# Kernel optimization log

Hardware: AMD Instinct MI355X
Metric: run time of the kernel (lower is better)

Reference implementation:

```python
import jax, jax.numpy as jnp
import numpy as np

NEG_INF = -9e15  # matches torch's -9000000000000000.0 fill


def setup_inputs() -> dict:
    key = jax.random.key(0)
    k1, k2, k3 = jax.random.split(key, 3)
    N, F = 8192, 256
    x = jax.random.normal(k1, (N, F), dtype=jnp.float32)
    adj = jax.random.randint(k2, (N, N), 0, 2, dtype=jnp.int32)
    # weight init mimics uniform(-stdv, stdv), stdv = 1/sqrt(F)
    stdv = 1.0 / np.sqrt(F)
    weight = jax.random.uniform(k3, (F, F), dtype=jnp.float32, minval=-stdv, maxval=stdv)
    return {"x": x, "adj": adj, "weight": weight}


def reference(x, adj, weight):
    # h: [N, F]
    h = x @ weight
    # e: [N, N] pairwise scores
    e = jnp.einsum("nf,mf->nm", h, h)
    masked = jnp.where(adj > 0, e, jnp.float32(NEG_INF))
    return jax.nn.softmax(masked, axis=1)
```

## Files before the change

kernel.cpp:

```cpp
#include <hip/hip_runtime.h>

typedef _Float16 f16;
typedef _Float16 f16x8 __attribute__((ext_vector_type(8)));
typedef float f32x4 __attribute__((ext_vector_type(4)));
typedef unsigned int u32;

#define NN 8192
#define FF 256
#define MASK_NEG -1.0e30f

__device__ __forceinline__ void gload_lds16(const void* gsrc, void* ldst) {
    __builtin_amdgcn_global_load_lds(
        (const __attribute__((address_space(1))) u32*)gsrc,
        (__attribute__((address_space(3))) u32*)ldst, 16, 0, 0);
}

__global__ void k0_wt(const float* __restrict__ w, f16* __restrict__ wt) {
    int n = blockIdx.x;
    int k = threadIdx.x;
    wt[n * FF + k] = (f16)w[k * FF + n];
}

__global__ __launch_bounds__(256) void k1_h(const float* __restrict__ x,
                                            const f16* __restrict__ wt,
                                            f16* __restrict__ h) {
    int tid = threadIdx.x;
    int wave = tid >> 6, lane = tid & 63, l15 = lane & 15, lg = lane >> 4;
    int rowBase = blockIdx.x * 32 + (wave & 1) * 16;
    int colBase = (wave >> 1) * 128;

    f16x8 afr[8];
    const float* xr = x + (size_t)(rowBase + l15) * FF + lg * 8;
#pragma unroll
    for (int kk = 0; kk < 8; ++kk) {
        float4 a0 = *(const float4*)(xr + kk * 32);
        float4 a1 = *(const float4*)(xr + kk * 32 + 4);
        f16x8 a;
        a[0] = (f16)a0.x; a[1] = (f16)a0.y; a[2] = (f16)a0.z; a[3] = (f16)a0.w;
        a[4] = (f16)a1.x; a[5] = (f16)a1.y; a[6] = (f16)a1.z; a[7] = (f16)a1.w;
        afr[kk] = a;
    }
#pragma unroll
    for (int cs = 0; cs < 8; ++cs) {
        int col = colBase + cs * 16 + l15;
        f32x4 acc = {0.f, 0.f, 0.f, 0.f};
        const f16* wr = wt + (size_t)col * FF + lg * 8;
#pragma unroll
        for (int kk = 0; kk < 8; ++kk) {
            f16x8 b = *(const f16x8*)(wr + kk * 32);
            acc = __builtin_amdgcn_mfma_f32_16x16x32_f16(afr[kk], b, acc, 0, 0, 0);
        }
#pragma unroll
        for (int r = 0; r < 4; ++r)
            h[(size_t)(rowBase + 4 * lg + r) * FF + col] = (f16)acc[r];
    }
}

__global__ __launch_bounds__(256) void k2a(const f16* __restrict__ h,
                                           const int* __restrict__ adj,
                                           u32* __restrict__ maskbits,
                                           float* __restrict__ pm,
                                           float* __restrict__ ps) {
    __shared__ __align__(16) f16 tile[128 * 256];
    int bid = blockIdx.x;
    int rb = bid >> 2, split = bid & 3;
    int tid = threadIdx.x;
    int wave = tid >> 6, lane = tid & 63, l15 = lane & 15, lg = lane >> 4;
    int rowBase = rb * 64 + wave * 16;

    f16x8 afr[8];
    {
        const f16* ar = h + (size_t)(rowBase + l15) * FF + lg * 8;
#pragma unroll
        for (int kk = 0; kk < 8; ++kk) afr[kk] = *(const f16x8*)(ar + kk * 32);
    }
    float m[4], s[4];
#pragma unroll
    for (int r = 0; r < 4; ++r) { m[r] = MASK_NEG; s[r] = 0.f; }

    int colStart = split * 2048;
    int prow = rowBase + (lane >> 2);
    int pwc = lane & 3;
    const int* adjRow = adj + (size_t)prow * NN;

    int4 aj[8];
    {
        const int4* ap = (const int4*)(adjRow + colStart + pwc * 32);
#pragma unroll
        for (int k = 0; k < 8; ++k) aj[k] = ap[k];
    }

    for (int it = 0; it < 16; ++it) {
        int c0 = colStart + it * 128;
        __syncthreads();
#pragma unroll
        for (int i = 0; i < 16; ++i) {
            int cbase = i * 256 + wave * 64;
            int c = cbase + lane;
            int row = c >> 5;
            int kb = (c & 31) * 16;
            const char* src = (const char*)h + (size_t)(c0 + row) * 512
                              + (kb ^ ((row & 7) << 4));
            gload_lds16(src, (char*)tile + (size_t)cbase * 16);
        }
        __syncthreads();

        u32 word = 0;
#pragma unroll
        for (int k = 0; k < 8; ++k) {
            word |= (aj[k].x > 0 ? 1u : 0u) << (k * 4);
            word |= (aj[k].y > 0 ? 1u : 0u) << (k * 4 + 1);
            word |= (aj[k].z > 0 ? 1u : 0u) << (k * 4 + 2);
            word |= (aj[k].w > 0 ? 1u : 0u) << (k * 4 + 3);
        }
        maskbits[(size_t)prow * 256 + (c0 >> 5) + pwc] = word;

        if (it + 1 < 16) {
            const int4* ap = (const int4*)(adjRow + c0 + 128 + pwc * 32);
#pragma unroll
            for (int k = 0; k < 8; ++k) aj[k] = ap[k];
        }

        f32x4 acc[8];
#pragma unroll
        for (int cs = 0; cs < 8; ++cs) {
            int trow = cs * 16 + l15;
            const char* tbase = (const char*)tile + trow * 512;
            int sw = (trow & 7) << 4;
            f32x4 a = {0.f, 0.f, 0.f, 0.f};
#pragma unroll
            for (int kk = 0; kk < 8; ++kk) {
                f16x8 b = *(const f16x8*)(tbase + ((kk * 64 + lg * 16) ^ sw));
                a = __builtin_amdgcn_mfma_f32_16x16x32_f16(afr[kk], b, a, 0, 0, 0);
            }
            acc[cs] = a;
        }

#pragma unroll
        for (int r = 0; r < 4; ++r) {
            int srcBase = 16 * lg + 4 * r;
            float vv[8];
            float tm = MASK_NEG;
#pragma unroll
            for (int wc = 0; wc < 4; ++wc) {
                u32 w = (u32)__shfl((int)word, srcBase + wc, 64);
                float v0 = ((w >> l15) & 1u) ? acc[wc * 2][r] : MASK_NEG;
                float v1 = ((w >> (16 + l15)) & 1u) ? acc[wc * 2 + 1][r] : MASK_NEG;
                vv[wc * 2] = v0;
                vv[wc * 2 + 1] = v1;
                tm = fmaxf(tm, fmaxf(v0, v1));
            }
            float mn = fmaxf(m[r], tm);
            float add = 0.f;
#pragma unroll
            for (int cs = 0; cs < 8; ++cs) add += __expf(vv[cs] - mn);
            s[r] = s[r] * __expf(m[r] - mn) + add;
            m[r] = mn;
        }
    }

#pragma unroll
    for (int off = 1; off < 16; off <<= 1) {
#pragma unroll
        for (int r = 0; r < 4; ++r) {
            float om = __shfl_xor(m[r], off);
            float os = __shfl_xor(s[r], off);
            float mn = fmaxf(m[r], om);
            s[r] = s[r] * __expf(m[r] - mn) + os * __expf(om - mn);
            m[r] = mn;
        }
    }
    if (l15 == 0) {
        int row0 = rowBase + 4 * lg;
#pragma unroll
        for (int r = 0; r < 4; ++r) {
            pm[split * NN + row0 + r] = m[r];
            ps[split * NN + row0 + r] = s[r];
        }
    }
}

__global__ void k2r(const float* __restrict__ pm, const float* __restrict__ ps,
                    float* __restrict__ fm, float* __restrict__ frs) {
    int row = blockIdx.x * 256 + threadIdx.x;
    float M = MASK_NEG, S = 0.f;
#pragma unroll
    for (int i = 0; i < 4; ++i) {
        float m = pm[i * NN + row];
        float s = ps[i * NN + row];
        float mn = fmaxf(M, m);
        S = S * __expf(M - mn) + s * __expf(m - mn);
        M = mn;
    }
    fm[row] = M;
    frs[row] = 1.0f / S;
}

__global__ __launch_bounds__(256) void k2b(const f16* __restrict__ h,
                                           const u32* __restrict__ maskbits,
                                           const float* __restrict__ fm,
                                           const float* __restrict__ frs,
                                           float* __restrict__ out) {
    __shared__ __align__(16) f16 tile[128 * 256];
    int cb = blockIdx.x;
    int rb = blockIdx.y;
    int tid = threadIdx.x;
    int wave = tid >> 6, lane = tid & 63, l15 = lane & 15, lg = lane >> 4;
    int rowBase = rb * 64 + wave * 16;
    int c0 = cb * 128;

#pragma unroll
    for (int i = 0; i < 16; ++i) {
        int cbase = i * 256 + wave * 64;
        int c = cbase + lane;
        int row = c >> 5;
        int kb = (c & 31) * 16;
        const char* src = (const char*)h + (size_t)(c0 + row) * 512
                          + (kb ^ ((row & 7) << 4));
        gload_lds16(src, (char*)tile + (size_t)cbase * 16);
    }

    u32 word = maskbits[(size_t)(rowBase + (lane >> 2)) * 256 + cb * 4 + (lane & 3)];

    f16x8 afr[8];
    const f16* ar = h + (size_t)(rowBase + l15) * FF + lg * 8;
#pragma unroll
    for (int kk = 0; kk < 8; ++kk) afr[kk] = *(const f16x8*)(ar + kk * 32);

    float M[4], RS[4];
#pragma unroll
    for (int r = 0; r < 4; ++r) {
        M[r] = fm[rowBase + 4 * lg + r];
        RS[r] = frs[rowBase + 4 * lg + r];
    }
    __syncthreads();

    f32x4 acc[8];
#pragma unroll
    for (int cs = 0; cs < 8; ++cs) {
        int trow = cs * 16 + l15;
        const char* tbase = (const char*)tile + trow * 512;
        int sw = (trow & 7) << 4;
        f32x4 a = {0.f, 0.f, 0.f, 0.f};
#pragma unroll
        for (int kk = 0; kk < 8; ++kk) {
            f16x8 b = *(const f16x8*)(tbase + ((kk * 64 + lg * 16) ^ sw));
            a = __builtin_amdgcn_mfma_f32_16x16x32_f16(afr[kk], b, a, 0, 0, 0);
        }
        acc[cs] = a;
    }

#pragma unroll
    for (int r = 0; r < 4; ++r) {
        int row = rowBase + 4 * lg + r;
        int srcBase = 16 * lg + 4 * r;
        float* orow = out + (size_t)row * NN + c0;
#pragma unroll
        for (int wc = 0; wc < 4; ++wc) {
            u32 w = (u32)__shfl((int)word, srcBase + wc, 64);
            float v0 = ((w >> l15) & 1u) ? acc[wc * 2][r] : MASK_NEG;
            float v1 = ((w >> (16 + l15)) & 1u) ? acc[wc * 2 + 1][r] : MASK_NEG;
            orow[wc * 32 + l15] = __expf(v0 - M[r]) * RS[r];
            orow[wc * 32 + 16 + l15] = __expf(v1 - M[r]) * RS[r];
        }
    }
}

extern "C" void kernel_launch(void* const* d_in, const int* in_sizes, int n_in,
                              void* d_out, int out_size, void* d_ws, size_t ws_size,
                              hipStream_t stream) {
    const float* x   = (const float*)d_in[0];
    const int*   adj = (const int*)d_in[1];
    const float* w   = (const float*)d_in[2];
    float* out = (float*)d_out;
    char* ws = (char*)d_ws;

    f16* h    = (f16*)(ws);
    f16* wt   = (f16*)(ws + 4194304);
    u32* mask = (u32*)(ws + 4194304 + 131072);
    float* pm = (float*)(ws + 4194304 + 131072 + 8388608);
    float* ps = pm + 4 * NN;
    float* fm = ps + 4 * NN;
    float* frs = fm + NN;

    k0_wt<<<dim3(256), dim3(256), 0, stream>>>(w, wt);
    k1_h <<<dim3(256), dim3(256), 0, stream>>>(x, wt, h);
    k2a  <<<dim3(512), dim3(256), 0, stream>>>(h, adj, mask, pm, ps);
    k2r  <<<dim3(32),  dim3(256), 0, stream>>>(pm, ps, fm, frs);
    k2b  <<<dim3(64, 128), dim3(256), 0, stream>>>(h, mask, fm, frs, out);
}
```

Before: 217.3 us.

## Split adjacency bit-packing into a standalone kernel ahead of score pass

Moves the conversion of the int32 adjacency matrix into a packed bitmask out of the k2a score/statistics kernel and into a dedicated fully parallel kpack kernel launched first. k2a now reads one packed word per iteration instead of streaming 128 bytes of adjacency per lane alongside its MFMA work. This is meant to let the adjacency read, the dominant memory traffic, run at full bandwidth across the whole GPU, and to relieve k2a of register pressure and interleaved global loads. The cost is an extra kernel launch and a serialization point, since the adjacency read no longer overlaps with compute.

```diff
diff --git a/kernel.cpp b/kernel.cpp
--- a/kernel.cpp
+++ b/kernel.cpp
@@ -56,9 +56,26 @@
     }
 }
 
+__global__ __launch_bounds__(256) void kpack(const int* __restrict__ adj,
+                                             u32* __restrict__ maskbits) {
+    int g = blockIdx.x * 256 + threadIdx.x;
+    const int4* ap = (const int4*)(adj + (size_t)g * 32);
+    int4 a[8];
+#pragma unroll
+    for (int k = 0; k < 8; ++k) a[k] = ap[k];
+    u32 word = 0;
+#pragma unroll
+    for (int k = 0; k < 8; ++k) {
+        word |= (a[k].x > 0 ? 1u : 0u) << (k * 4);
+        word |= (a[k].y > 0 ? 1u : 0u) << (k * 4 + 1);
+        word |= (a[k].z > 0 ? 1u : 0u) << (k * 4 + 2);
+        word |= (a[k].w > 0 ? 1u : 0u) << (k * 4 + 3);
+    }
+    maskbits[g] = word;
+}
+
 __global__ __launch_bounds__(256) void k2a(const f16* __restrict__ h,
-                                           const int* __restrict__ adj,
-                                           u32* __restrict__ maskbits,
+                                           const u32* __restrict__ maskbits,
                                            float* __restrict__ pm,
                                            float* __restrict__ ps) {
     __shared__ __align__(16) f16 tile[128 * 256];
@@ -79,16 +96,7 @@
     for (int r = 0; r < 4; ++r) { m[r] = MASK_NEG; s[r] = 0.f; }
 
     int colStart = split * 2048;
-    int prow = rowBase + (lane >> 2);
-    int pwc = lane & 3;
-    const int* adjRow = adj + (size_t)prow * NN;
-
-    int4 aj[8];
-    {
-        const int4* ap = (const int4*)(adjRow + colStart + pwc * 32);
-#pragma unroll
-        for (int k = 0; k < 8; ++k) aj[k] = ap[k];
-    }
+    const u32* mrow = maskbits + (size_t)(rowBase + (lane >> 2)) * 256 + (lane & 3);
 
     for (int it = 0; it < 16; ++it) {
         int c0 = colStart + it * 128;
@@ -103,23 +111,8 @@
                               + (kb ^ ((row & 7) << 4));
             gload_lds16(src, (char*)tile + (size_t)cbase * 16);
         }
+        u32 word = mrow[c0 >> 5];
         __syncthreads();
-
-        u32 word = 0;
-#pragma unroll
-        for (int k = 0; k < 8; ++k) {
-            word |= (aj[k].x > 0 ? 1u : 0u) << (k * 4);
-            word |= (aj[k].y > 0 ? 1u : 0u) << (k * 4 + 1);
-            word |= (aj[k].z > 0 ? 1u : 0u) << (k * 4 + 2);
-            word |= (aj[k].w > 0 ? 1u : 0u) << (k * 4 + 3);
-        }
-        maskbits[(size_t)prow * 256 + (c0 >> 5) + pwc] = word;
-
-        if (it + 1 < 16) {
-            const int4* ap = (const int4*)(adjRow + c0 + 128 + pwc * 32);
-#pragma unroll
-            for (int k = 0; k < 8; ++k) aj[k] = ap[k];
-        }
 
         f32x4 acc[8];
 #pragma unroll
@@ -283,9 +276,10 @@
     float* fm = ps + 4 * NN;
     float* frs = fm + NN;
 
+    kpack<<<dim3(8192), dim3(256), 0, stream>>>(adj, mask);
     k0_wt<<<dim3(256), dim3(256), 0, stream>>>(w, wt);
     k1_h <<<dim3(256), dim3(256), 0, stream>>>(x, wt, h);
-    k2a  <<<dim3(512), dim3(256), 0, stream>>>(h, adj, mask, pm, ps);
+    k2a  <<<dim3(512), dim3(256), 0, stream>>>(h, mask, pm, ps);
     k2r  <<<dim3(32),  dim3(256), 0, stream>>>(pm, ps, fm, frs);
     k2b  <<<dim3(64, 128), dim3(256), 0, stream>>>(h, mask, fm, frs, out);
 }
```

Result: slower. 231.5 us (+6.6%).
